# Performance work log

Measured on AMD Instinct MI355X. Metric: run time of the kernel, lower is better.

## Reference

```python
import jax, jax.numpy as jnp
import numpy as np

WEIGHT = 0.1
SIGMA_RGB = 15.0
SIGMA_XY = 80.0
SCALE = 0.5
IGNORE_LABEL = 255


def _resize_bilinear(x, oh, ow):
    # PyTorch F.interpolate(mode='bilinear', align_corners=False): half-pixel centers.
    H, W = x.shape[-2], x.shape[-1]
    def coords(o, i):
        c = jnp.clip((jnp.arange(o, dtype=x.dtype) + 0.5) * (i / o) - 0.5, 0.0, i - 1.0)
        i0 = jnp.floor(c).astype(jnp.int32)
        i1 = jnp.minimum(i0 + 1, i - 1)
        return i0, i1, c - i0.astype(x.dtype)
    y0, y1, wy = coords(oh, H)
    x0, x1, wx = coords(ow, W)
    r0 = x[..., y0, :]
    r1 = x[..., y1, :]
    top = r0[..., x0] * (1.0 - wx) + r0[..., x1] * wx
    bot = r1[..., x0] * (1.0 - wx) + r1[..., x1] * wx
    return top * (1.0 - wy)[:, None] + bot * wy[:, None]


def _resize_nearest(x, oh, ow):
    # PyTorch F.interpolate(mode='nearest'): src = floor(dst * in/out).
    H, W = x.shape[-2], x.shape[-1]
    yi = jnp.floor(jnp.arange(oh) * (H / oh)).astype(jnp.int32)
    xi = jnp.floor(jnp.arange(ow) * (W / ow)).astype(jnp.int32)
    return x[..., yi, :][..., xi]


def _dense_energy(images, segmentations, ROIs, seg_label):
    N, K, H, W = segmentations.shape
    oh, ow = int(H * SCALE), int(W * SCALE)
    P = oh * ow

    img_s = _resize_nearest(images, oh, ow)             # [N,3,oh,ow]
    seg_s = _resize_bilinear(segmentations, oh, ow)     # [N,K,oh,ow]
    roi_s = _resize_nearest(ROIs[:, None], oh, ow)[:, 0]  # [N,oh,ow]
    lab_s = _resize_nearest(seg_label, oh, ow)          # [N,1,oh,ow]

    unlabel = (jax.lax.stop_gradient(lab_s).astype(jnp.int32) == IGNORE_LABEL)[:, 0]
    gate = roi_s - jnp.max(seg_s, axis=1)               # ROI - max_k seg
    gate = jnp.where(unlabel, 1.0, gate)
    gate = jax.lax.stop_gradient(jnp.maximum(gate, 0.0))  # [N,oh,ow], constant in bwd

    seg_m = (seg_s * roi_s[:, None]).reshape(N, K, P)   # ROI-masked probs [N,K,P]

    # Bilateral features: (x/sxy, y/sxy, r/srgb, g/srgb, b/srgb); sxy scaled by SCALE as in forward().
    sxy = SIGMA_XY * SCALE
    ys, xs = jnp.meshgrid(jnp.arange(oh, dtype=images.dtype),
                          jnp.arange(ow, dtype=images.dtype), indexing='ij')
    xy = jnp.stack([xs.ravel(), ys.ravel()], axis=1) / sxy          # [P,2]
    rgb = img_s.reshape(N, 3, P).transpose(0, 2, 1) / SIGMA_RGB      # [N,P,3]
    feat = jnp.concatenate([jnp.broadcast_to(xy, (N, P, 2)), rgb], axis=-1)  # [N,P,5]

    def filt_one(f, s):
        # f: [P,5] features, s: [K,P] masked probs -> Gaussian-filtered probs [K,P]
        sq = jnp.sum(f * f, axis=-1)                                 # [P]
        d2 = jnp.maximum(sq[:, None] + sq[None, :] - 2.0 * (f @ f.T), 0.0)
        A = jnp.exp(-0.5 * d2)                                       # dense exact kernel [P,P]
        return jnp.einsum('pq,kq->kp', A, s)

    AS = jax.vmap(filt_one)(feat, seg_m)                # [N,K,P]
    gate_f = gate.reshape(N, 1, P)
    loss = -0.5 * jnp.sum(seg_m * gate_f * AS) / (N * P)
    return WEIGHT * loss


def setup_inputs() -> dict:
    key = jax.random.key(0)
    k1, k2, k3 = jax.random.split(key, 3)
    N, K, H, W = 4, 21, 128, 128
    images = jax.random.uniform(k1, (N, 3, H, W), dtype=jnp.float32) * 255.0
    segs = jax.random.uniform(k2, (N, K, H, W), dtype=jnp.float32)
    segs = segs / jnp.sum(segs, axis=1, keepdims=True)  # prob-like
    ROIs = jnp.ones((N, H, W), dtype=jnp.float32)
    seg_label = jax.random.randint(k3, (N, 1, H, W), 0, 256).astype(jnp.float32)
    return {'images': images, 'segmentations': segs, 'ROIs': ROIs, 'seg_label': seg_label}


def reference(images, segmentations, ROIs, seg_label):
    return _dense_energy(images, segmentations, ROIs, seg_label)
```

## Files before the change

kernel.cpp:

```cpp
#include <hip/hip_runtime.h>
#include <hip/hip_bf16.h>


constexpr int N_ = 4, K_ = 21, H_ = 128, W_ = 128, P_ = 4096;
constexpr int T_ = 128;
constexpr int NT = P_ / T_;
constexpr int NTRI = NT * (NT + 1) / 2;
constexpr int NBLK = NTRI * N_;
constexpr float INV_RGB = 1.0f / 15.0f;
constexpr float INV_XY = 1.0f / 40.0f;
constexpr float LOG2E = 1.4426950408889634f;
constexpr float NEG_HALF_LOG2E = -0.72134752044448170f;
constexpr float OUT_SCALE = -0.05f / 16384.0f;

typedef _Float16 half8 __attribute__((ext_vector_type(8)));
typedef float floatx4 __attribute__((ext_vector_type(4)));


__global__ void __launch_bounds__(256) prep_kernel(
    const float* __restrict__ img, const float* __restrict__ seg,
    const float* __restrict__ roi, const float* __restrict__ lab,
    _Float16* __restrict__ segh, _Float16* __restrict__ feath,
    float2* __restrict__ scal) {
  int idx = blockIdx.x * 256 + threadIdx.x;
  int n = idx >> 12;
  int p = idx & (P_ - 1);
  int y = p >> 6, x = p & 63;
  int iy = 2 * y, ix = 2 * x;
  const size_t hw = (size_t)H_ * W_;

  float r = roi[(size_t)n * hw + iy * W_ + ix];
  float lb = lab[(size_t)n * hw + iy * W_ + ix];
  bool unlabeled = ((int)lb == 255);

  const float* sb = seg + (size_t)n * K_ * hw + (size_t)iy * W_ + ix;
  _Float16 sh[32];
  float mx = -1e30f;
#pragma unroll
  for (int k = 0; k < K_; k++) {
    const float* s = sb + (size_t)k * hw;
    float v = 0.25f * (s[0] + s[1] + s[W_] + s[W_ + 1]);
    mx = fmaxf(mx, v);
    sh[k] = (_Float16)(v * r);
  }
#pragma unroll
  for (int k = K_; k < 32; k++) sh[k] = (_Float16)0.0f;

  const float* ib = img + (size_t)n * 3 * hw + (size_t)iy * W_ + ix;
  _Float16 fh[8];
  fh[0] = (_Float16)((float)x * INV_XY);
  fh[1] = (_Float16)((float)y * INV_XY);
  fh[2] = (_Float16)(ib[0] * INV_RGB);
  fh[3] = (_Float16)(ib[hw] * INV_RGB);
  fh[4] = (_Float16)(ib[2 * hw] * INV_RGB);
  fh[5] = (_Float16)0.0f; fh[6] = (_Float16)0.0f; fh[7] = (_Float16)0.0f;
  float sq = 0.0f;
#pragma unroll
  for (int j = 0; j < 5; j++) { float v = (float)fh[j]; sq = fmaf(v, v, sq); }

  float4* sdst = (float4*)(segh + (size_t)idx * 32);
  const float4* ssrc = (const float4*)sh;
#pragma unroll
  for (int j = 0; j < 4; j++) sdst[j] = ssrc[j];
  *(float4*)(feath + (size_t)idx * 8) = *(const float4*)fh;

  float g = unlabeled ? 1.0f : (r - mx);
  scal[idx] = make_float2(NEG_HALF_LOG2E * sq, fmaxf(g, 0.0f));
}

__global__ void __launch_bounds__(256) energy_kernel(
    const _Float16* __restrict__ segh, const _Float16* __restrict__ feath,
    const float2* __restrict__ scal, float* __restrict__ partial) {
  int t = blockIdx.x;
  int pb = 0;
  while (t >= NT - pb) { t -= NT - pb; pb++; }
  int qb = pb + t;
  int n = blockIdx.y;
  int tid = threadIdx.x;
  int lane = tid & 63, wave = tid >> 6;
  int m = lane & 15, quad = lane >> 4;

  const _Float16* segn = segh + (size_t)n * P_ * 32;
  const _Float16* featn = feath + (size_t)n * P_ * 8;
  const float2* scaln = scal + (size_t)n * P_;

  __shared__ float2 sp_[T_], sq_[T_];
  for (int i = tid; i < T_; i += 256) {
    sp_[i] = scaln[pb * T_ + i];
    sq_[i] = scaln[qb * T_ + i];
  }
  __syncthreads();

  half8 aseg[2], afeat[2];
  const half8 zfrag = {};
#pragma unroll
  for (int s = 0; s < 2; s++) {
    int prow = pb * T_ + (2 * wave + s) * 16 + m;
    aseg[s] = *(const half8*)(segn + (size_t)prow * 32 + quad * 8);
    half8 f = *(const half8*)(featn + (size_t)prow * 8);
    afeat[s] = (quad == 0) ? f : zfrag;
  }
  float cspv[2][4], gpv[2][4];
#pragma unroll
  for (int s = 0; s < 2; s++)
#pragma unroll
    for (int r = 0; r < 4; r++) {
      float2 tpr = sp_[(2 * wave + s) * 16 + quad * 4 + r];
      cspv[s][r] = tpr.x; gpv[s][r] = tpr.y;
    }

  float acc = 0.0f;
#pragma unroll 2
  for (int qs = 0; qs < 8; qs++) {
    int qrow = qb * T_ + qs * 16 + m;
    half8 bseg = *(const half8*)(segn + (size_t)qrow * 32 + quad * 8);
    half8 bf = *(const half8*)(featn + (size_t)qrow * 8);
    half8 bfeat = (quad == 0) ? bf : zfrag;
    float2 qsc = sq_[qs * 16 + m];
#pragma unroll
    for (int s = 0; s < 2; s++) {
      floatx4 G = {0.0f, 0.0f, 0.0f, 0.0f};
      floatx4 D = {0.0f, 0.0f, 0.0f, 0.0f};
      G = __builtin_amdgcn_mfma_f32_16x16x32_f16(aseg[s], bseg, G, 0, 0, 0);
      D = __builtin_amdgcn_mfma_f32_16x16x32_f16(afeat[s], bfeat, D, 0, 0, 0);
#pragma unroll
      for (int r = 0; r < 4; r++) {
        float arg = fmaf(LOG2E, D[r], cspv[s][r] + qsc.x);
        float A = __builtin_amdgcn_exp2f(arg);
        A = fminf(A, 1.0f);
        acc = fmaf(A * G[r], gpv[s][r] + qsc.y, acc);
      }
    }
  }

#pragma unroll
  for (int off = 32; off > 0; off >>= 1) acc += __shfl_down(acc, off, 64);
  __shared__ float wsum[4];
  if (lane == 0) wsum[wave] = acc;
  __syncthreads();
  if (tid == 0) {
    float s = (wsum[0] + wsum[1]) + (wsum[2] + wsum[3]);
    float wb = (pb == qb) ? 0.5f : 1.0f;
    partial[blockIdx.y * NTRI + blockIdx.x] = s * wb;
  }
}

__global__ void __launch_bounds__(256) reduce_kernel(
    const float* __restrict__ partial, float* __restrict__ out) {
  int tid = threadIdx.x;
  float acc = 0.0f;
  for (int i = tid; i < NBLK; i += 256) acc += partial[i];
#pragma unroll
  for (int off = 32; off > 0; off >>= 1) acc += __shfl_down(acc, off, 64);
  __shared__ float wsum[4];
  int lane = tid & 63, wave = tid >> 6;
  if (lane == 0) wsum[wave] = acc;
  __syncthreads();
  if (tid == 0) {
    float s = (wsum[0] + wsum[1]) + (wsum[2] + wsum[3]);
    out[0] = s * OUT_SCALE;
  }
}

extern "C" void kernel_launch(void* const* d_in, const int* in_sizes, int n_in,
                              void* d_out, int out_size, void* d_ws, size_t ws_size,
                              hipStream_t stream) {
  const float* images = (const float*)d_in[0];
  const float* segs = (const float*)d_in[1];
  const float* rois = (const float*)d_in[2];
  const float* labels = (const float*)d_in[3];
  float* out = (float*)d_out;

  char* ws = (char*)d_ws;
  _Float16* segh = (_Float16*)ws;
  _Float16* feath = (_Float16*)(ws + (size_t)N_ * P_ * 32 * 2);
  float2* scal = (float2*)(ws + (size_t)N_ * P_ * 32 * 2 + (size_t)N_ * P_ * 8 * 2);
  float* partial = (float*)(ws + (size_t)N_ * P_ * 32 * 2 + (size_t)N_ * P_ * 8 * 2 +
                            (size_t)N_ * P_ * sizeof(float2));

  prep_kernel<<<dim3(N_ * P_ / 256), dim3(256), 0, stream>>>(
      images, segs, rois, labels, segh, feath, scal);
  energy_kernel<<<dim3(NTRI, N_), dim3(256), 0, stream>>>(segh, feath, scal, partial);
  reduce_kernel<<<dim3(1), dim3(256), 0, stream>>>(partial, out);
}
```

Baseline: 84.23 us.

## Pack seg and feature channels into one 32-wide row, derive dot by subtraction

Packs the 21 segmentation channels and the 5 bilateral features into a single 32-half row per pixel, so one global load feeds both MFMAs. The feature dot product is obtained as the full-row MFMA minus the seg-only MFMA (the A operand with its feature quad zeroed), which drops the separate feature buffer and its loads. It also preloads all eight B fragments and the per-q scalars into registers and removes the shared-memory staging and the __syncthreads. The trade-offs are higher register pressure and extra fp16 cancellation error in the subtraction-derived distance.

```diff
diff --git a/kernel.cpp b/kernel.cpp
--- a/kernel.cpp
+++ b/kernel.cpp
@@ -20,8 +20,7 @@
 __global__ void __launch_bounds__(256) prep_kernel(
     const float* __restrict__ img, const float* __restrict__ seg,
     const float* __restrict__ roi, const float* __restrict__ lab,
-    _Float16* __restrict__ segh, _Float16* __restrict__ feath,
-    float2* __restrict__ scal) {
+    _Float16* __restrict__ comb, float2* __restrict__ scal) {
   int idx = blockIdx.x * 256 + threadIdx.x;
   int n = idx >> 12;
   int p = idx & (P_ - 1);
@@ -34,43 +33,41 @@
   bool unlabeled = ((int)lb == 255);
 
   const float* sb = seg + (size_t)n * K_ * hw + (size_t)iy * W_ + ix;
-  _Float16 sh[32];
+  _Float16 ch[32];
   float mx = -1e30f;
 #pragma unroll
   for (int k = 0; k < K_; k++) {
     const float* s = sb + (size_t)k * hw;
     float v = 0.25f * (s[0] + s[1] + s[W_] + s[W_ + 1]);
     mx = fmaxf(mx, v);
-    sh[k] = (_Float16)(v * r);
+    ch[k] = (_Float16)(v * r);
   }
-#pragma unroll
-  for (int k = K_; k < 32; k++) sh[k] = (_Float16)0.0f;
+  ch[21] = (_Float16)0.0f; ch[22] = (_Float16)0.0f; ch[23] = (_Float16)0.0f;
 
   const float* ib = img + (size_t)n * 3 * hw + (size_t)iy * W_ + ix;
-  _Float16 fh[8];
-  fh[0] = (_Float16)((float)x * INV_XY);
-  fh[1] = (_Float16)((float)y * INV_XY);
-  fh[2] = (_Float16)(ib[0] * INV_RGB);
-  fh[3] = (_Float16)(ib[hw] * INV_RGB);
-  fh[4] = (_Float16)(ib[2 * hw] * INV_RGB);
-  fh[5] = (_Float16)0.0f; fh[6] = (_Float16)0.0f; fh[7] = (_Float16)0.0f;
+  ch[24] = (_Float16)((float)x * INV_XY);
+  ch[25] = (_Float16)((float)y * INV_XY);
+  ch[26] = (_Float16)(ib[0] * INV_RGB);
+  ch[27] = (_Float16)(ib[hw] * INV_RGB);
+  ch[28] = (_Float16)(ib[2 * hw] * INV_RGB);
+  ch[29] = (_Float16)0.0f; ch[30] = (_Float16)0.0f; ch[31] = (_Float16)0.0f;
+
   float sq = 0.0f;
 #pragma unroll
-  for (int j = 0; j < 5; j++) { float v = (float)fh[j]; sq = fmaf(v, v, sq); }
+  for (int j = 24; j < 29; j++) { float v = (float)ch[j]; sq = fmaf(v, v, sq); }
 
-  float4* sdst = (float4*)(segh + (size_t)idx * 32);
-  const float4* ssrc = (const float4*)sh;
+  float4* dst = (float4*)(comb + (size_t)idx * 32);
+  const float4* src = (const float4*)ch;
 #pragma unroll
-  for (int j = 0; j < 4; j++) sdst[j] = ssrc[j];
-  *(float4*)(feath + (size_t)idx * 8) = *(const float4*)fh;
+  for (int j = 0; j < 4; j++) dst[j] = src[j];
 
   float g = unlabeled ? 1.0f : (r - mx);
   scal[idx] = make_float2(NEG_HALF_LOG2E * sq, fmaxf(g, 0.0f));
 }
 
 __global__ void __launch_bounds__(256) energy_kernel(
-    const _Float16* __restrict__ segh, const _Float16* __restrict__ feath,
-    const float2* __restrict__ scal, float* __restrict__ partial) {
+    const _Float16* __restrict__ comb, const float2* __restrict__ scal,
+    float* __restrict__ partial) {
   int t = blockIdx.x;
   int pb = 0;
   while (t >= NT - pb) { t -= NT - pb; pb++; }
@@ -80,55 +77,51 @@
   int lane = tid & 63, wave = tid >> 6;
   int m = lane & 15, quad = lane >> 4;
 
-  const _Float16* segn = segh + (size_t)n * P_ * 32;
-  const _Float16* featn = feath + (size_t)n * P_ * 8;
+  const _Float16* combn = comb + (size_t)n * P_ * 32;
   const float2* scaln = scal + (size_t)n * P_;
+  const half8 zfrag = {};
 
-  __shared__ float2 sp_[T_], sq_[T_];
-  for (int i = tid; i < T_; i += 256) {
-    sp_[i] = scaln[pb * T_ + i];
-    sq_[i] = scaln[qb * T_ + i];
-  }
-  __syncthreads();
-
-  half8 aseg[2], afeat[2];
-  const half8 zfrag = {};
+  half8 acomb[2], aseg0[2];
 #pragma unroll
   for (int s = 0; s < 2; s++) {
     int prow = pb * T_ + (2 * wave + s) * 16 + m;
-    aseg[s] = *(const half8*)(segn + (size_t)prow * 32 + quad * 8);
-    half8 f = *(const half8*)(featn + (size_t)prow * 8);
-    afeat[s] = (quad == 0) ? f : zfrag;
+    acomb[s] = *(const half8*)(combn + (size_t)prow * 32 + quad * 8);
+    aseg0[s] = (quad == 3) ? zfrag : acomb[s];
   }
+  half8 bcomb[8];
+#pragma unroll
+  for (int qs = 0; qs < 8; qs++) {
+    int qrow = qb * T_ + qs * 16 + m;
+    bcomb[qs] = *(const half8*)(combn + (size_t)qrow * 32 + quad * 8);
+  }
+  float2 qsc[8];
+#pragma unroll
+  for (int qs = 0; qs < 8; qs++) qsc[qs] = scaln[qb * T_ + qs * 16 + m];
   float cspv[2][4], gpv[2][4];
 #pragma unroll
   for (int s = 0; s < 2; s++)
 #pragma unroll
     for (int r = 0; r < 4; r++) {
-      float2 tpr = sp_[(2 * wave + s) * 16 + quad * 4 + r];
+      float2 tpr = scaln[pb * T_ + (2 * wave + s) * 16 + quad * 4 + r];
       cspv[s][r] = tpr.x; gpv[s][r] = tpr.y;
     }
 
   float acc = 0.0f;
 #pragma unroll 2
   for (int qs = 0; qs < 8; qs++) {
-    int qrow = qb * T_ + qs * 16 + m;
-    half8 bseg = *(const half8*)(segn + (size_t)qrow * 32 + quad * 8);
-    half8 bf = *(const half8*)(featn + (size_t)qrow * 8);
-    half8 bfeat = (quad == 0) ? bf : zfrag;
-    float2 qsc = sq_[qs * 16 + m];
 #pragma unroll
     for (int s = 0; s < 2; s++) {
+      floatx4 C1 = {0.0f, 0.0f, 0.0f, 0.0f};
       floatx4 G = {0.0f, 0.0f, 0.0f, 0.0f};
-      floatx4 D = {0.0f, 0.0f, 0.0f, 0.0f};
-      G = __builtin_amdgcn_mfma_f32_16x16x32_f16(aseg[s], bseg, G, 0, 0, 0);
-      D = __builtin_amdgcn_mfma_f32_16x16x32_f16(afeat[s], bfeat, D, 0, 0, 0);
+      C1 = __builtin_amdgcn_mfma_f32_16x16x32_f16(acomb[s], bcomb[qs], C1, 0, 0, 0);
+      G = __builtin_amdgcn_mfma_f32_16x16x32_f16(aseg0[s], bcomb[qs], G, 0, 0, 0);
 #pragma unroll
       for (int r = 0; r < 4; r++) {
-        float arg = fmaf(LOG2E, D[r], cspv[s][r] + qsc.x);
+        float dot = C1[r] - G[r];
+        float arg = fmaf(LOG2E, dot, cspv[s][r] + qsc[qs].x);
         float A = __builtin_amdgcn_exp2f(arg);
         A = fminf(A, 1.0f);
-        acc = fmaf(A * G[r], gpv[s][r] + qsc.y, acc);
+        acc = fmaf(A * G[r], gpv[s][r] + qsc[qs].y, acc);
       }
     }
   }
@@ -172,14 +165,13 @@
   float* out = (float*)d_out;
 
   char* ws = (char*)d_ws;
-  _Float16* segh = (_Float16*)ws;
-  _Float16* feath = (_Float16*)(ws + (size_t)N_ * P_ * 32 * 2);
-  float2* scal = (float2*)(ws + (size_t)N_ * P_ * 32 * 2 + (size_t)N_ * P_ * 8 * 2);
-  float* partial = (float*)(ws + (size_t)N_ * P_ * 32 * 2 + (size_t)N_ * P_ * 8 * 2 +
+  _Float16* comb = (_Float16*)ws;
+  float2* scal = (float2*)(ws + (size_t)N_ * P_ * 32 * 2);
+  float* partial = (float*)(ws + (size_t)N_ * P_ * 32 * 2 +
                             (size_t)N_ * P_ * sizeof(float2));
 
   prep_kernel<<<dim3(N_ * P_ / 256), dim3(256), 0, stream>>>(
-      images, segs, rois, labels, segh, feath, scal);
-  energy_kernel<<<dim3(NTRI, N_), dim3(256), 0, stream>>>(segh, feath, scal, partial);
+      images, segs, rois, labels, comb, scal);
+  energy_kernel<<<dim3(NTRI, N_), dim3(256), 0, stream>>>(comb, scal, partial);
   reduce_kernel<<<dim3(1), dim3(256), 0, stream>>>(partial, out);
 }
```

New measurement: 330.6 us. 293% more time.
